# Kernel tuning notes

Hardware: AMD Instinct MI355X
Metric: run time of the kernel (lower is better)

The kernel has to match this reference:

```python
import jax, jax.numpy as jnp
import numpy as np

NUM_HEADS = 16


def setup_inputs() -> dict:
    key = jax.random.key(0)
    ks = jax.random.split(key, 9)
    B, N, C, R, T = 16, 1024, 1024, 64, 10
    s = 0.02
    x = jax.random.normal(ks[0], (B, N, C), dtype=jnp.float32)
    W_qkv = jax.random.normal(ks[1], (3 * C, C), dtype=jnp.float32) * s
    W_proj = jax.random.normal(ks[2], (C, C), dtype=jnp.float32) * s
    b_proj = jax.random.normal(ks[3], (C,), dtype=jnp.float32) * s
    A_k = jax.random.normal(ks[4], (T, R, C), dtype=jnp.float32) * s
    B_k = jax.random.normal(ks[5], (T, C, R), dtype=jnp.float32) * s
    A_v = jax.random.normal(ks[6], (T, R, C), dtype=jnp.float32) * s
    B_v = jax.random.normal(ks[7], (T, C, R), dtype=jnp.float32) * s
    return {"x": x, "W_qkv": W_qkv, "W_proj": W_proj, "b_proj": b_proj,
            "A_k": A_k, "B_k": B_k, "A_v": A_v, "B_v": B_v, "task": 4}


def reference(x, W_qkv, W_proj, b_proj, A_k, B_k, A_v, B_v, task):
    B, N, C = x.shape
    H = NUM_HEADS
    hd = C // H
    scale = hd ** (-0.5)

    # qkv projection: x @ W_qkv.T -> [B,N,3C] -> [3,B,H,N,hd]
    qkv = (x @ W_qkv.T).reshape(B, N, 3, H, hd).transpose(2, 0, 3, 1, 4)
    q, k, v = qkv[0], qkv[1], qkv[2]

    # merged LoRA weights: sum_{t<=task} B[t] @ A[t] -> [C, C]
    w_k = jnp.einsum('tcr,trd->cd', B_k[:task + 1], A_k[:task + 1])
    w_v = jnp.einsum('tcr,trd->cd', B_v[:task + 1], A_v[:task + 1])
    # F.linear(x, W) = x @ W.T ; reshape to [B,H,N,hd]
    dk = (x @ w_k.T).reshape(B, N, H, hd).transpose(0, 2, 1, 3)
    dv = (x @ w_v.T).reshape(B, N, H, hd).transpose(0, 2, 1, 3)
    k = k + dk
    v = v + dv

    attn = jax.nn.softmax(jnp.einsum('bhnd,bhmd->bhnm', q, k) * scale, axis=-1)
    out = jnp.einsum('bhnm,bhmd->bhnd', attn, v)
    out = out.transpose(0, 2, 1, 3).reshape(B, N, C)
    return out @ W_proj.T + b_proj
```

## Files before the change

### kernel.cpp

```cpp
#include <hip/hip_runtime.h>

typedef __attribute__((ext_vector_type(4))) float f32x4;
typedef __attribute__((ext_vector_type(8))) short s16x8;
typedef __attribute__((ext_vector_type(2))) unsigned int u32x2;
typedef __attribute__((ext_vector_type(4))) unsigned int u32x4;

#define LOG2E 1.44269504088896340736f

__device__ inline unsigned short f2b(float f) {
  unsigned int u = __float_as_uint(f);
  unsigned int r = (u + 0x7FFFu + ((u >> 16) & 1u)) >> 16;
  return (unsigned short)r;
}

__device__ inline unsigned int cvtpk_bf16(float lo, float hi) {
  unsigned int r;
  asm("v_cvt_pk_bf16_f32 %0, %1, %2" : "=v"(r) : "v"(lo), "v"(hi));
  return r;
}

__device__ inline void gload_lds16(const unsigned short* g, unsigned short* l) {
  __builtin_amdgcn_global_load_lds(
      (const __attribute__((address_space(1))) unsigned int*)g,
      (__attribute__((address_space(3))) unsigned int*)l, 16, 0, 0);
}

__global__ __launch_bounds__(256) void lora_merge(const float* __restrict__ A_k,
                                                  const float* __restrict__ B_k,
                                                  const float* __restrict__ A_v,
                                                  const float* __restrict__ B_v,
                                                  float* __restrict__ wk,
                                                  float* __restrict__ wv,
                                                  const int* __restrict__ taskp) {
  const float* A_ = blockIdx.y ? A_v : A_k;
  const float* B_ = blockIdx.y ? B_v : B_k;
  float* Wd = blockIdx.y ? wv : wk;
  __shared__ float Bs[64][65];
  __shared__ float As[64][65];
  const int tile = blockIdx.x;
  const int c0 = (tile >> 4) * 64, d0 = (tile & 15) * 64;
  const int tid = threadIdx.x;
  const int tx = tid & 15, ty = tid >> 4;
  const int T = *taskp + 1;
  float acc[4][4] = {};
  const int r = tid >> 2, cb = (tid & 3) * 16;
  for (int t = 0; t < T; ++t) {
    __syncthreads();
    const float* srcB = B_ + (size_t)t * 65536 + (size_t)(c0 + r) * 64 + cb;
    const float* srcA = A_ + (size_t)t * 65536 + (size_t)r * 1024 + d0 + cb;
#pragma unroll
    for (int j = 0; j < 16; j += 4) {
      f32x4 vb = *(const f32x4*)(srcB + j);
      Bs[r][cb + j] = vb.x; Bs[r][cb + j + 1] = vb.y;
      Bs[r][cb + j + 2] = vb.z; Bs[r][cb + j + 3] = vb.w;
      f32x4 va = *(const f32x4*)(srcA + j);
      As[r][cb + j] = va.x; As[r][cb + j + 1] = va.y;
      As[r][cb + j + 2] = va.z; As[r][cb + j + 3] = va.w;
    }
    __syncthreads();
#pragma unroll 8
    for (int rr = 0; rr < 64; ++rr) {
      float bv[4], av[4];
#pragma unroll
      for (int i = 0; i < 4; ++i) bv[i] = Bs[ty * 4 + i][rr];
#pragma unroll
      for (int j = 0; j < 4; ++j) av[j] = As[rr][tx * 4 + j];
#pragma unroll
      for (int i = 0; i < 4; ++i)
#pragma unroll
        for (int j = 0; j < 4; ++j) acc[i][j] += bv[i] * av[j];
    }
  }
#pragma unroll
  for (int i = 0; i < 4; ++i)
#pragma unroll
    for (int j = 0; j < 4; ++j)
      Wd[(size_t)(c0 + ty * 4 + i) * 1024 + d0 + tx * 4 + j] = acc[i][j];
}

__global__ void prep_cvt(const float* __restrict__ x, const float* __restrict__ Wproj,
                         unsigned short* __restrict__ xb, unsigned short* __restrict__ Wp) {
  int i = blockIdx.x * 256 + threadIdx.x;
  const float* src;
  unsigned short* dst;
  int idx;
  if (i < 4194304) { src = x; dst = xb; idx = i; }
  else { idx = i - 4194304; if (idx >= 262144) return; src = Wproj; dst = Wp; }
  f32x4 v = ((const f32x4*)src)[idx];
  unsigned short o0 = f2b(v.x), o1 = f2b(v.y), o2 = f2b(v.z), o3 = f2b(v.w);
  unsigned long long pack = (unsigned long long)o0 | ((unsigned long long)o1 << 16) |
                            ((unsigned long long)o2 << 32) | ((unsigned long long)o3 << 48);
  ((unsigned long long*)dst)[idx] = pack;
}

__global__ void build_wc(const float* __restrict__ Wqkv, const float* __restrict__ wk,
                         const float* __restrict__ wv, unsigned short* __restrict__ Wc) {
  int i = blockIdx.x * 256 + threadIdx.x;
  int e = i * 4;
  f32x4 v = *(const f32x4*)(Wqkv + e);
  int row = e >> 10;
  if (row >= 2048) {
    f32x4 d = *(const f32x4*)(wv + (e - 2097152));
    v = v + d;
  } else if (row >= 1024) {
    f32x4 d = *(const f32x4*)(wk + (e - 1048576));
    v = v + d;
  }
  unsigned short o0 = f2b(v.x), o1 = f2b(v.y), o2 = f2b(v.z), o3 = f2b(v.w);
  unsigned long long pack = (unsigned long long)o0 | ((unsigned long long)o1 << 16) |
                            ((unsigned long long)o2 << 32) | ((unsigned long long)o3 << 48);
  ((unsigned long long*)Wc)[i] = pack;
}

template <int OUT_BF16, int ADD_BIAS>
__global__ __launch_bounds__(512, 1) void gemm256(const unsigned short* __restrict__ A,
                                                  const unsigned short* __restrict__ B,
                                                  void* __restrict__ Cout,
                                                  const float* __restrict__ bias,
                                                  int M, int N, int K) {
  __shared__ unsigned short SA[4][8192];
  __shared__ unsigned short SB[4][8192];
  const int tid = threadIdx.x;
  const int w = tid >> 6, l = tid & 63;
  const int lr = l & 15, lg = l >> 4;
  const int wm = w >> 2, wn = w & 3;

  const int lin = blockIdx.y * gridDim.x + blockIdx.x;
  const int cpx = (gridDim.x * gridDim.y) >> 3;
  const int s = (lin & 7) * cpx + (lin >> 3);
  const int bx = s % gridDim.x, by = s / gridDim.x;

  const int cs = tid ^ (((tid >> 5) & 1) << 1);
  const int r_st = ((cs >> 6) << 4) | ((cs >> 2) & 15);
  const int k_st = (cs & 3) << 3;
  const unsigned short* gA0 = A + (size_t)(by * 256 + r_st) * K + k_st;
  const unsigned short* gA1 = A + (size_t)(by * 256 + 128 + r_st) * K + k_st;
  const unsigned short* gB0 = B + (size_t)(bx * 256 + r_st) * K + k_st;
  const unsigned short* gB1 = B + (size_t)(bx * 256 + 128 + r_st) * K + k_st;
  const int wb = w * 512;

  const int swz = ((lr >> 3) & 1) << 4;
  const int fbase = lr * 32 + lg * 8;
  const int hA = wm * 4096;
  const int hB = (wn >> 1) * 4096;
  const int nb = (wn & 1) * 4;

  f32x4 acc[8][4] = {};
  const int NT = K >> 5;

#pragma unroll
  for (int t = 0; t < 3; ++t) {
    gload_lds16(gA0 + t * 32, &SA[t][wb]);
    gload_lds16(gA1 + t * 32, &SA[t][4096 + wb]);
    gload_lds16(gB0 + t * 32, &SB[t][wb]);
    gload_lds16(gB1 + t * 32, &SB[t][4096 + wb]);
  }
  asm volatile("s_waitcnt vmcnt(8)" ::: "memory");
  __builtin_amdgcn_s_barrier();
  __builtin_amdgcn_sched_barrier(0);

  for (int t = 0; t < NT; ++t) {
    const int slot = t & 3;
    const int ts = (t + 3 < NT) ? (t + 3) : (NT - 1);
    const int ssl = (t + 3) & 3;
    const unsigned short* sa = &SA[slot][hA];
    const unsigned short* sb = &SB[slot][hB];
    s16x8 af[8], bf[2];
#pragma unroll
    for (int m = 0; m < 8; ++m)
      af[m] = *(const s16x8*)&sa[(m * 512 + fbase) ^ swz];
#pragma unroll
    for (int n = 0; n < 2; ++n)
      bf[n] = *(const s16x8*)&sb[((nb + n) * 512 + fbase) ^ swz];
    gload_lds16(gA0 + ts * 32, &SA[ssl][wb]);
    gload_lds16(gA1 + ts * 32, &SA[ssl][4096 + wb]);
    __builtin_amdgcn_s_barrier();
    asm volatile("s_waitcnt lgkmcnt(0)" ::: "memory");
    __builtin_amdgcn_sched_barrier(0);
    __builtin_amdgcn_s_setprio(1);
#pragma unroll
    for (int m = 0; m < 8; ++m)
#pragma unroll
      for (int n = 0; n < 2; ++n)
        acc[m][n] = __builtin_amdgcn_mfma_f32_16x16x32_bf16(af[m], bf[n], acc[m][n], 0, 0, 0);
    __builtin_amdgcn_s_setprio(0);
    __builtin_amdgcn_sched_barrier(0);
    __builtin_amdgcn_s_barrier();
#pragma unroll
    for (int n = 0; n < 2; ++n)
      bf[n] = *(const s16x8*)&sb[((nb + 2 + n) * 512 + fbase) ^ swz];
    gload_lds16(gB0 + ts * 32, &SB[ssl][wb]);
    gload_lds16(gB1 + ts * 32, &SB[ssl][4096 + wb]);
    __builtin_amdgcn_s_barrier();
    asm volatile("s_waitcnt lgkmcnt(0)" ::: "memory");
    __builtin_amdgcn_sched_barrier(0);
    __builtin_amdgcn_s_setprio(1);
#pragma unroll
    for (int m = 0; m < 8; ++m)
#pragma unroll
      for (int n = 0; n < 2; ++n)
        acc[m][2 + n] = __builtin_amdgcn_mfma_f32_16x16x32_bf16(af[m], bf[n], acc[m][2 + n], 0, 0, 0);
    __builtin_amdgcn_s_setprio(0);
    __builtin_amdgcn_sched_barrier(0);
    asm volatile("s_waitcnt vmcnt(8)" ::: "memory");
    __builtin_amdgcn_s_barrier();
    __builtin_amdgcn_sched_barrier(0);
  }

  const int crow0 = by * 256 + wm * 128;
  const int ccol0 = bx * 256 + wn * 64;
  if (OUT_BF16) {
    unsigned short* C = (unsigned short*)Cout;
#pragma unroll
    for (int m = 0; m < 8; ++m)
#pragma unroll
      for (int n = 0; n < 4; ++n)
#pragma unroll
        for (int rr = 0; rr < 4; ++rr) {
          int row = crow0 + m * 16 + lg * 4 + rr;
          int col = ccol0 + n * 16 + lr;
          C[(size_t)row * N + col] = f2b(acc[m][n][rr]);
        }
  } else {
    float* C = (float*)Cout;
#pragma unroll
    for (int m = 0; m < 8; ++m)
#pragma unroll
      for (int n = 0; n < 4; ++n)
#pragma unroll
        for (int rr = 0; rr < 4; ++rr) {
          int row = crow0 + m * 16 + lg * 4 + rr;
          int col = ccol0 + n * 16 + lr;
          float b = ADD_BIAS ? bias[col] : 0.f;
          C[(size_t)row * N + col] = acc[m][n][rr] + b;
        }
  }
}

__global__ __launch_bounds__(64) void transpose_v(const unsigned short* __restrict__ qkv,
                                                  unsigned short* __restrict__ vT) {
  __shared__ unsigned short T[64 * 65];
  const int bh = blockIdx.x >> 4;
  const int nt = blockIdx.x & 15;
  const int b = bh >> 4, h = bh & 15;
  const int l = threadIdx.x;
  const unsigned short* src = qkv + (size_t)(b * 1024 + nt * 64) * 3072 + 2048 + h * 64;
#pragma unroll
  for (int p = 0; p < 8; ++p) {
    int slot = p * 64 + l;
    int n = slot >> 3, dc = (slot & 7) * 8;
    u32x4 v = *(const u32x4*)(src + (size_t)n * 3072 + dc);
    const unsigned short* vs = (const unsigned short*)&v;
#pragma unroll
    for (int j = 0; j < 8; ++j) T[n * 65 + dc + j] = vs[j];
  }
  __syncthreads();
  unsigned short* dst = vT + (size_t)bh * 65536 + nt * 64;
#pragma unroll
  for (int p = 0; p < 8; ++p) {
    int slot = p * 64 + l;
    int d = slot >> 3, nc = (slot & 7) * 8;
    union { unsigned short s[8]; u32x4 v; } tmp;
#pragma unroll
    for (int j = 0; j < 8; ++j) tmp.s[j] = T[(nc + j) * 65 + d];
    *(u32x4*)(dst + (size_t)d * 1024 + nc) = tmp.v;
  }
}

__global__ __launch_bounds__(512) void attn_fwd(const unsigned short* __restrict__ qkv,
                                                const unsigned short* __restrict__ vT,
                                                unsigned short* __restrict__ out) {
  const int tid = threadIdx.x;
  const int w = tid >> 6, l = tid & 63;
  const int lr = l & 15, lg = l >> 4;
  const int bid = blockIdx.x;
  const int g = ((bid >> 6) << 3) | (bid & 7);
  const int qt = (bid >> 3) & 7;
  const int b = g >> 4, h = g & 15;

  __shared__ unsigned short Ks[2][4096];
  __shared__ unsigned short Vs[2][4096];
  __shared__ unsigned int Ps[8][576];

  const size_t base = (size_t)b * 1024 * 3072 + h * 64;
  const unsigned short* Qp = qkv + base;
  const unsigned short* Kp = qkv + base + 1024;
  const unsigned short* vTp = vT + (size_t)(b * 16 + h) * 65536;

  const float SSCALE = 0.125f * LOG2E;
  const int qrow = qt * 128 + w * 16 + lr;
  s16x8 qf[2];
  qf[0] = *(const s16x8*)(Qp + (size_t)qrow * 3072 + lg * 8);
  qf[1] = *(const s16x8*)(Qp + (size_t)qrow * 3072 + 32 + lg * 8);
#pragma unroll
  for (int kk = 0; kk < 2; ++kk)
#pragma unroll
    for (int j = 0; j < 8; ++j) {
      float f = __uint_as_float(((unsigned int)(unsigned short)qf[kk][j]) << 16) * SSCALE;
      qf[kk][j] = (short)f2b(f);
    }

  f32x4 o[4] = {};
  float lrun = 0.f;

  const int srow = tid >> 3;
  const int csrc = (tid & 7) ^ (srow & 7);

  gload_lds16(Kp + (size_t)srow * 3072 + csrc * 8, &Ks[0][w * 512]);
  gload_lds16(vTp + (size_t)srow * 1024 + csrc * 8, &Vs[0][w * 512]);
  __syncthreads();

  for (int t = 0; t < 16; ++t) {
    const int cur = t & 1;
    if (t < 15) {
      const int kv1 = (t + 1) * 64;
      gload_lds16(Kp + (size_t)(kv1 + srow) * 3072 + csrc * 8, &Ks[cur ^ 1][w * 512]);
      gload_lds16(vTp + (size_t)srow * 1024 + kv1 + csrc * 8, &Vs[cur ^ 1][w * 512]);
    }
    const unsigned short* Kb = &Ks[cur][0];
    const unsigned short* Vb = &Vs[cur][0];

    f32x4 sc[4];
#pragma unroll
    for (int tt = 0; tt < 4; ++tt) {
      f32x4 a = {0.f, 0.f, 0.f, 0.f};
#pragma unroll
      for (int kk = 0; kk < 2; ++kk) {
        int krow = tt * 16 + lr;
        s16x8 kf = *(const s16x8*)&Kb[krow * 64 + ((((kk * 32 + lg * 8) >> 3) ^ (krow & 7)) << 3)];
        a = __builtin_amdgcn_mfma_f32_16x16x32_bf16(kf, qf[kk], a, 0, 0, 0);
      }
      sc[tt] = a;
    }

#pragma unroll
    for (int tt = 0; tt < 4; ++tt) {
      float p0 = exp2f(sc[tt][0]);
      float p1 = exp2f(sc[tt][1]);
      float p2 = exp2f(sc[tt][2]);
      float p3 = exp2f(sc[tt][3]);
      lrun += (p0 + p1) + (p2 + p3);
      u32x2 pk;
      pk.x = cvtpk_bf16(p0, p1);
      pk.y = cvtpk_bf16(p2, p3);
      *(u32x2*)&Ps[w][lr * 36 + tt * 8 + lg * 2] = pk;
    }
    __builtin_amdgcn_sched_barrier(0);

#pragma unroll
    for (int kk = 0; kk < 2; ++kk) {
      u32x4 pu = *(const u32x4*)&Ps[w][lr * 36 + kk * 16 + lg * 4];
      s16x8 pf = __builtin_bit_cast(s16x8, pu);
#pragma unroll
      for (int dt = 0; dt < 4; ++dt) {
        int vrow = dt * 16 + lr;
        s16x8 vf = *(const s16x8*)&Vb[vrow * 64 + ((((kk * 32 + lg * 8) >> 3) ^ (vrow & 7)) << 3)];
        o[dt] = __builtin_amdgcn_mfma_f32_16x16x32_bf16(pf, vf, o[dt], 0, 0, 0);
      }
    }
    __syncthreads();
  }

  lrun += __shfl_xor(lrun, 16);
  lrun += __shfl_xor(lrun, 32);
  float lq[4];
#pragma unroll
  for (int rr = 0; rr < 4; ++rr) lq[rr] = 1.f / __shfl(lrun, lg * 4 + rr);

  const size_t orow0 = (size_t)b * 1024 + qt * 128 + w * 16;
#pragma unroll
  for (int dt = 0; dt < 4; ++dt)
#pragma unroll
    for (int rr = 0; rr < 4; ++rr)
      out[(orow0 + lg * 4 + rr) * 1024 + h * 64 + dt * 16 + lr] = f2b(o[dt][rr] * lq[rr]);
}

extern "C" void kernel_launch(void* const* d_in, const int* in_sizes, int n_in,
                              void* d_out, int out_size, void* d_ws, size_t ws_size,
                              hipStream_t stream) {
  const float* x = (const float*)d_in[0];
  const float* Wqkv = (const float*)d_in[1];
  const float* Wproj = (const float*)d_in[2];
  const float* bproj = (const float*)d_in[3];
  const float* A_k = (const float*)d_in[4];
  const float* B_k = (const float*)d_in[5];
  const float* A_v = (const float*)d_in[6];
  const float* B_v = (const float*)d_in[7];
  const int* task = (const int*)d_in[8];

  char* ws = (char*)d_ws;
  float* wk = (float*)ws;
  float* wv = (float*)(ws + (4ull << 20));
  unsigned short* xb = (unsigned short*)(ws + (8ull << 20));
  unsigned short* Wc = (unsigned short*)(ws + (40ull << 20));
  unsigned short* Wp = (unsigned short*)(ws + (46ull << 20));
  unsigned short* qkv = (unsigned short*)(ws + (48ull << 20));
  unsigned short* ao = (unsigned short*)(ws + (144ull << 20));
  unsigned short* vT = xb;

  lora_merge<<<dim3(256, 2), 256, 0, stream>>>(A_k, B_k, A_v, B_v, wk, wv, task);
  prep_cvt<<<17408, 256, 0, stream>>>(x, Wproj, xb, Wp);
  build_wc<<<3072, 256, 0, stream>>>(Wqkv, wk, wv, Wc);
  gemm256<1, 0><<<dim3(12, 64), 512, 0, stream>>>(xb, Wc, qkv, nullptr, 16384, 3072, 1024);
  transpose_v<<<4096, 64, 0, stream>>>(qkv, vT);
  attn_fwd<<<2048, 512, 0, stream>>>(qkv, vT, ao);
  gemm256<0, 1><<<dim3(4, 64), 512, 0, stream>>>(ao, Wp, d_out, bproj, 16384, 1024, 1024);
}
```

Measured before the change: 328.4 us.

## Process two query tiles per attention block to reuse K/V loads

```diff
diff --git a/kernel.cpp b/kernel.cpp
--- a/kernel.cpp
+++ b/kernel.cpp
@@ -274,13 +274,13 @@
   const int w = tid >> 6, l = tid & 63;
   const int lr = l & 15, lg = l >> 4;
   const int bid = blockIdx.x;
-  const int g = ((bid >> 6) << 3) | (bid & 7);
-  const int qt = (bid >> 3) & 7;
+  const int g = (bid & 7) * 32 + (bid >> 5);
+  const int qt2 = (bid >> 3) & 3;
   const int b = g >> 4, h = g & 15;
 
   __shared__ unsigned short Ks[2][4096];
   __shared__ unsigned short Vs[2][4096];
-  __shared__ unsigned int Ps[8][576];
+  __shared__ unsigned int Ps[16][576];
 
   const size_t base = (size_t)b * 1024 * 3072 + h * 64;
   const unsigned short* Qp = qkv + base;
@@ -288,20 +288,24 @@
   const unsigned short* vTp = vT + (size_t)(b * 16 + h) * 65536;
 
   const float SSCALE = 0.125f * LOG2E;
-  const int qrow = qt * 128 + w * 16 + lr;
-  s16x8 qf[2];
-  qf[0] = *(const s16x8*)(Qp + (size_t)qrow * 3072 + lg * 8);
-  qf[1] = *(const s16x8*)(Qp + (size_t)qrow * 3072 + 32 + lg * 8);
-#pragma unroll
-  for (int kk = 0; kk < 2; ++kk)
-#pragma unroll
-    for (int j = 0; j < 8; ++j) {
-      float f = __uint_as_float(((unsigned int)(unsigned short)qf[kk][j]) << 16) * SSCALE;
-      qf[kk][j] = (short)f2b(f);
-    }
-
-  f32x4 o[4] = {};
-  float lrun = 0.f;
+  const int qb = qt2 * 256;
+  s16x8 qf[2][2];
+#pragma unroll
+  for (int qg = 0; qg < 2; ++qg) {
+    const int qrow = qb + qg * 128 + w * 16 + lr;
+    qf[qg][0] = *(const s16x8*)(Qp + (size_t)qrow * 3072 + lg * 8);
+    qf[qg][1] = *(const s16x8*)(Qp + (size_t)qrow * 3072 + 32 + lg * 8);
+#pragma unroll
+    for (int kk = 0; kk < 2; ++kk)
+#pragma unroll
+      for (int j = 0; j < 8; ++j) {
+        float f = __uint_as_float(((unsigned int)(unsigned short)qf[qg][kk][j]) << 16) * SSCALE;
+        qf[qg][kk][j] = (short)f2b(f);
+      }
+  }
+
+  f32x4 o[2][4] = {};
+  float lrun[2] = {0.f, 0.f};
 
   const int srow = tid >> 3;
   const int csrc = (tid & 7) ^ (srow & 7);
@@ -320,59 +324,66 @@
     const unsigned short* Kb = &Ks[cur][0];
     const unsigned short* Vb = &Vs[cur][0];
 
-    f32x4 sc[4];
-#pragma unroll
-    for (int tt = 0; tt < 4; ++tt) {
-      f32x4 a = {0.f, 0.f, 0.f, 0.f};
+#pragma unroll
+    for (int qg = 0; qg < 2; ++qg) {
+      unsigned int* Pw = &Ps[(w << 1) | qg][0];
+      f32x4 sc[4];
+#pragma unroll
+      for (int tt = 0; tt < 4; ++tt) {
+        f32x4 a = {0.f, 0.f, 0.f, 0.f};
+#pragma unroll
+        for (int kk = 0; kk < 2; ++kk) {
+          int krow = tt * 16 + lr;
+          s16x8 kf = *(const s16x8*)&Kb[krow * 64 + ((((kk * 32 + lg * 8) >> 3) ^ (krow & 7)) << 3)];
+          a = __builtin_amdgcn_mfma_f32_16x16x32_bf16(kf, qf[qg][kk], a, 0, 0, 0);
+        }
+        sc[tt] = a;
+      }
+
+#pragma unroll
+      for (int tt = 0; tt < 4; ++tt) {
+        float p0 = exp2f(sc[tt][0]);
+        float p1 = exp2f(sc[tt][1]);
+        float p2 = exp2f(sc[tt][2]);
+        float p3 = exp2f(sc[tt][3]);
+        lrun[qg] += (p0 + p1) + (p2 + p3);
+        u32x2 pk;
+        pk.x = cvtpk_bf16(p0, p1);
+        pk.y = cvtpk_bf16(p2, p3);
+        *(u32x2*)&Pw[lr * 36 + tt * 8 + lg * 2] = pk;
+      }
+      __builtin_amdgcn_sched_barrier(0);
+
 #pragma unroll
       for (int kk = 0; kk < 2; ++kk) {
-        int krow = tt * 16 + lr;
-        s16x8 kf = *(const s16x8*)&Kb[krow * 64 + ((((kk * 32 + lg * 8) >> 3) ^ (krow & 7)) << 3)];
-        a = __builtin_amdgcn_mfma_f32_16x16x32_bf16(kf, qf[kk], a, 0, 0, 0);
-      }
-      sc[tt] = a;
-    }
-
-#pragma unroll
-    for (int tt = 0; tt < 4; ++tt) {
-      float p0 = exp2f(sc[tt][0]);
-      float p1 = exp2f(sc[tt][1]);
-      float p2 = exp2f(sc[tt][2]);
-      float p3 = exp2f(sc[tt][3]);
-      lrun += (p0 + p1) + (p2 + p3);
-      u32x2 pk;
-      pk.x = cvtpk_bf16(p0, p1);
-      pk.y = cvtpk_bf16(p2, p3);
-      *(u32x2*)&Ps[w][lr * 36 + tt * 8 + lg * 2] = pk;
-    }
-    __builtin_amdgcn_sched_barrier(0);
-
-#pragma unroll
-    for (int kk = 0; kk < 2; ++kk) {
-      u32x4 pu = *(const u32x4*)&Ps[w][lr * 36 + kk * 16 + lg * 4];
-      s16x8 pf = __builtin_bit_cast(s16x8, pu);
-#pragma unroll
-      for (int dt = 0; dt < 4; ++dt) {
-        int vrow = dt * 16 + lr;
-        s16x8 vf = *(const s16x8*)&Vb[vrow * 64 + ((((kk * 32 + lg * 8) >> 3) ^ (vrow & 7)) << 3)];
-        o[dt] = __builtin_amdgcn_mfma_f32_16x16x32_bf16(pf, vf, o[dt], 0, 0, 0);
+        u32x4 pu = *(const u32x4*)&Pw[lr * 36 + kk * 16 + lg * 4];
+        s16x8 pf = __builtin_bit_cast(s16x8, pu);
+#pragma unroll
+        for (int dt = 0; dt < 4; ++dt) {
+          int vrow = dt * 16 + lr;
+          s16x8 vf = *(const s16x8*)&Vb[vrow * 64 + ((((kk * 32 + lg * 8) >> 3) ^ (vrow & 7)) << 3)];
+          o[qg][dt] = __builtin_amdgcn_mfma_f32_16x16x32_bf16(pf, vf, o[qg][dt], 0, 0, 0);
+        }
       }
     }
     __syncthreads();
   }
 
-  lrun += __shfl_xor(lrun, 16);
-  lrun += __shfl_xor(lrun, 32);
-  float lq[4];
-#pragma unroll
-  for (int rr = 0; rr < 4; ++rr) lq[rr] = 1.f / __shfl(lrun, lg * 4 + rr);
-
-  const size_t orow0 = (size_t)b * 1024 + qt * 128 + w * 16;
-#pragma unroll
-  for (int dt = 0; dt < 4; ++dt)
-#pragma unroll
-    for (int rr = 0; rr < 4; ++rr)
-      out[(orow0 + lg * 4 + rr) * 1024 + h * 64 + dt * 16 + lr] = f2b(o[dt][rr] * lq[rr]);
+#pragma unroll
+  for (int qg = 0; qg < 2; ++qg) {
+    float lr2 = lrun[qg];
+    lr2 += __shfl_xor(lr2, 16);
+    lr2 += __shfl_xor(lr2, 32);
+    float lq[4];
+#pragma unroll
+    for (int rr = 0; rr < 4; ++rr) lq[rr] = 1.f / __shfl(lr2, lg * 4 + rr);
+    const size_t orow0 = (size_t)b * 1024 + qb + qg * 128 + w * 16;
+#pragma unroll
+    for (int dt = 0; dt < 4; ++dt)
+#pragma unroll
+      for (int rr = 0; rr < 4; ++rr)
+        out[(orow0 + lg * 4 + rr) * 1024 + h * 64 + dt * 16 + lr] = f2b(o[qg][dt][rr] * lq[rr]);
+  }
 }
 
 extern "C" void kernel_launch(void* const* d_in, const int* in_sizes, int n_in,
@@ -403,6 +414,6 @@
   build_wc<<<3072, 256, 0, stream>>>(Wqkv, wk, wv, Wc);
   gemm256<1, 0><<<dim3(12, 64), 512, 0, stream>>>(xb, Wc, qkv, nullptr, 16384, 3072, 1024);
   transpose_v<<<4096, 64, 0, stream>>>(qkv, vT);
-  attn_fwd<<<2048, 512, 0, stream>>>(qkv, vT, ao);
+  attn_fwd<<<1024, 512, 0, stream>>>(qkv, vT, ao);
   gemm256<0, 1><<<dim3(4, 64), 512, 0, stream>>>(ao, Wp, d_out, bproj, 16384, 1024, 1024);
 }
```

New measurement: 341.3 us. +3.9%, slower.
